# Kernel tuning notes

Measured on AMD Instinct MI355X. Metric: run time of the kernel, lower is better.

## Reference

```python
import jax, jax.numpy as jnp
import numpy as np

H = 128          # input spatial size forced by hardcoded reshape (8 * 16)
BATCH = 128
BLK = 8          # block_size
SUB = 16         # out_channels (sub-frames)
WIN = 3          # window


def setup_inputs() -> dict:
    key = jax.random.key(0)
    k1, k2 = jax.random.split(key, 2)
    coded = jax.random.normal(k1, (BATCH, 1, H, H), dtype=jnp.float32)
    # Conv3d weight: [out=16*64, in/groups=1, kD=9, 1, 1]; kaiming-like scale sqrt(2/9)
    weight = jax.random.normal(k2, (SUB * BLK * BLK, 1, WIN * WIN, 1, 1), dtype=jnp.float32) * np.sqrt(2.0 / 9.0).astype(np.float32)
    bias = jnp.zeros((SUB * BLK * BLK,), dtype=jnp.float32)
    return {"coded": coded, "weight": weight, "bias": bias}


def reference(coded, weight, bias):
    N = coded.shape[0]
    # --- window_shuffle: conv with 3x3 identity filters, pad 1 == 9 shifted copies ---
    pad = jnp.pad(coded, ((0, 0), (0, 0), (1, 1), (1, 1)))  # [N,1,H+2,H+2]
    patches = jnp.stack(
        [pad[:, 0, i:i + H, j:j + H] for i in range(WIN) for j in range(WIN)],
        axis=1,
    )  # [N,9,H,H]
    # --- reverse_pixel_shuffle (space-to-depth, block 8), vectorized over the 9 channels ---
    Hs = H // BLK  # 16
    x = patches.reshape(N, WIN * WIN, Hs, BLK, Hs, BLK)
    x = x.transpose(0, 1, 3, 5, 2, 4).reshape(N, WIN * WIN, BLK * BLK, Hs, Hs)
    x = x.transpose(0, 2, 1, 3, 4)  # [N,64,9,16,16] (torch.stack dim=2 order)
    # --- depthwise Conv3d: groups=64, kernel (9,1,1) -> per-group 9-tap dot ---
    W = weight.reshape(BLK * BLK, SUB, WIN * WIN)  # [64,16,9]
    b = bias.reshape(BLK * BLK, SUB)               # [64,16]
    out = jnp.einsum('ngihw,gmi->ngmhw', x, W) + b[None, :, :, None, None]  # [N,64,16,16,16]
    # --- reshape/transpose/pixel-shuffle ---
    out = out.transpose(0, 2, 1, 3, 4).reshape(N, SUB * BLK * BLK, Hs, Hs)  # [N,1024,16,16]
    out = out.reshape(N, SUB, BLK, BLK, Hs, Hs)
    out = out.transpose(0, 1, 4, 2, 5, 3).reshape(N, SUB, H, H)  # [N,16,128,128]
    return out
```

## Files before the change

### kernel.cpp

```cpp
#include <hip/hip_runtime.h>


#define H 128
#define N_BATCH 128
#define SUB 16

__global__ __launch_bounds__(256, 4) void shiftconv_kernel(
        const float* __restrict__ x,
        const float* __restrict__ w,
        const float* __restrict__ bias,
        float* __restrict__ out) {
    int bid = blockIdx.x;
    int nlo = bid & 7;
    int q   = bid >> 3;
    int mh  = q & 1;
    int b1  = (q >> 1) & 7;
    int n   = ((q >> 4) << 3) | nlo;

    __shared__ float ws[8 * 80];
    {
        int t = threadIdx.x;
        if (t < 64) {
            int mi = t >> 3;
            int h  = (t >> 2) & 1;
            int jj = t & 3;
            int oc = (b1 * 8 + 4 * h + jj) * 16 + (mh * 8 + mi);
            float* dst = ws + mi * 80 + h * 40;
            const float* src = w + oc * 9;
#pragma unroll
            for (int i = 0; i < 9; ++i) dst[i * 4 + jj] = src[i];
            dst[36 + jj] = bias[oc];
        }
    }

    int c  = threadIdx.x & 31;
    int r  = threadIdx.x >> 5;
    int x0 = c << 2;
    int h  = c & 1;
    int y0 = b1 + (r << 3);

    const float* xn = x + (size_t)n * (H * H);

    float in[2][3][6];
#pragma unroll
    for (int g = 0; g < 2; ++g) {
        int yg = y0 + (g << 6);
#pragma unroll
        for (int dy = 0; dy < 3; ++dy) {
            int ry = yg + dy - 1;
            float4 a = make_float4(0.0f, 0.0f, 0.0f, 0.0f);
            if (ry >= 0 && ry < H) a = *(const float4*)(xn + ry * H + x0);
            in[g][dy][1] = a.x; in[g][dy][2] = a.y;
            in[g][dy][3] = a.z; in[g][dy][4] = a.w;
            float left  = __shfl_up(a.w, 1);
            float right = __shfl_down(a.x, 1);
            in[g][dy][0] = (c == 0)  ? 0.0f : left;
            in[g][dy][5] = (c == 31) ? 0.0f : right;
        }
    }

    __syncthreads();

    float* ob = out + ((size_t)(n * SUB + mh * 8)) * (H * H) + y0 * H + x0;

#pragma unroll
    for (int mi = 0; mi < 8; ++mi) {
        const float4* wp = (const float4*)(ws + mi * 80 + h * 40);
        float4 b4 = wp[9];
        float a0[4] = {b4.x, b4.y, b4.z, b4.w};
        float a1[4] = {b4.x, b4.y, b4.z, b4.w};
#pragma unroll
        for (int dy = 0; dy < 3; ++dy) {
#pragma unroll
            for (int dj = 0; dj < 3; ++dj) {
                float4 w4 = wp[dy * 3 + dj];
                a0[0] = fmaf(in[0][dy][dj + 0], w4.x, a0[0]);
                a0[1] = fmaf(in[0][dy][dj + 1], w4.y, a0[1]);
                a0[2] = fmaf(in[0][dy][dj + 2], w4.z, a0[2]);
                a0[3] = fmaf(in[0][dy][dj + 3], w4.w, a0[3]);
                a1[0] = fmaf(in[1][dy][dj + 0], w4.x, a1[0]);
                a1[1] = fmaf(in[1][dy][dj + 1], w4.y, a1[1]);
                a1[2] = fmaf(in[1][dy][dj + 2], w4.z, a1[2]);
                a1[3] = fmaf(in[1][dy][dj + 3], w4.w, a1[3]);
            }
        }
        float* p = ob + (size_t)mi * (H * H);
        *(float4*)(p)          = make_float4(a0[0], a0[1], a0[2], a0[3]);
        *(float4*)(p + 64 * H) = make_float4(a1[0], a1[1], a1[2], a1[3]);
    }
}

extern "C" void kernel_launch(void* const* d_in, const int* in_sizes, int n_in,
                              void* d_out, int out_size, void* d_ws, size_t ws_size,
                              hipStream_t stream) {
    const float* coded  = (const float*)d_in[0];
    const float* weight = (const float*)d_in[1];
    const float* bias   = (const float*)d_in[2];
    float* out = (float*)d_out;

    shiftconv_kernel<<<N_BATCH * 8 * 2, 256, 0, stream>>>(coded, weight, bias, out);
}
```

Measured before the change: 146.1 us.

## Prepack weights in a prep kernel and give each block contiguous rows

A small prep kernel repacks the weights and bias once into a workspace in the per-thread float4 layout. The main kernel then copies all 8 row-phase weight sets with coalesced float4 loads instead of scattered scalar gathers. Each block now covers 8 contiguous rows rather than rows strided by 8, so input loads and output stores are more contiguous. The costs are an extra kernel launch, larger shared memory per block (20KB), and each warp reading a different weight slice.

```diff
diff --git a/kernel.cpp b/kernel.cpp
--- a/kernel.cpp
+++ b/kernel.cpp
@@ -5,39 +5,48 @@
 #define N_BATCH 128
 #define SUB 16
 
+__global__ void wprep_kernel(const float* __restrict__ w,
+                             const float* __restrict__ bias,
+                             float* __restrict__ Wt) {
+    int t = blockIdx.x * blockDim.x + threadIdx.x;
+    if (t >= 1024) return;
+    int jj = t & 3;
+    int h  = (t >> 2) & 1;
+    int mi = (t >> 3) & 7;
+    int b1 = (t >> 6) & 7;
+    int mh = (t >> 9) & 1;
+    int oc = (b1 * 8 + 4 * h + jj) * 16 + mh * 8 + mi;
+    float* dst = Wt + ((mh * 8 + b1) * 8 + mi) * 80 + h * 40;
+#pragma unroll
+    for (int i = 0; i < 9; ++i) dst[i * 4 + jj] = w[oc * 9 + i];
+    dst[36 + jj] = bias[oc];
+}
+
 __global__ __launch_bounds__(256, 4) void shiftconv_kernel(
         const float* __restrict__ x,
-        const float* __restrict__ w,
-        const float* __restrict__ bias,
+        const float* __restrict__ Wt,
         float* __restrict__ out) {
     int bid = blockIdx.x;
     int nlo = bid & 7;
     int q   = bid >> 3;
     int mh  = q & 1;
-    int b1  = (q >> 1) & 7;
+    int k0  = (q >> 1) & 7;
     int n   = ((q >> 4) << 3) | nlo;
 
-    __shared__ float ws[8 * 80];
+    __shared__ float ws[8 * 8 * 80];
     {
         int t = threadIdx.x;
-        if (t < 64) {
-            int mi = t >> 3;
-            int h  = (t >> 2) & 1;
-            int jj = t & 3;
-            int oc = (b1 * 8 + 4 * h + jj) * 16 + (mh * 8 + mi);
-            float* dst = ws + mi * 80 + h * 40;
-            const float* src = w + oc * 9;
+        const float4* src = (const float4*)(Wt + mh * (8 * 8 * 80));
+        float4* dst = (float4*)ws;
 #pragma unroll
-            for (int i = 0; i < 9; ++i) dst[i * 4 + jj] = src[i];
-            dst[36 + jj] = bias[oc];
-        }
+        for (int i = 0; i < 5; ++i) dst[t + 256 * i] = src[t + 256 * i];
     }
 
     int c  = threadIdx.x & 31;
     int r  = threadIdx.x >> 5;
     int x0 = c << 2;
     int h  = c & 1;
-    int y0 = b1 + (r << 3);
+    int y0 = (k0 << 3) + r;
 
     const float* xn = x + (size_t)n * (H * H);
 
@@ -62,10 +71,11 @@
     __syncthreads();
 
     float* ob = out + ((size_t)(n * SUB + mh * 8)) * (H * H) + y0 * H + x0;
+    const float* wbase = ws + (r * 8) * 80 + h * 40;
 
 #pragma unroll
     for (int mi = 0; mi < 8; ++mi) {
-        const float4* wp = (const float4*)(ws + mi * 80 + h * 40);
+        const float4* wp = (const float4*)(wbase + mi * 80);
         float4 b4 = wp[9];
         float a0[4] = {b4.x, b4.y, b4.z, b4.w};
         float a1[4] = {b4.x, b4.y, b4.z, b4.w};
@@ -97,6 +107,8 @@
     const float* weight = (const float*)d_in[1];
     const float* bias   = (const float*)d_in[2];
     float* out = (float*)d_out;
+    float* Wt  = (float*)d_ws;
 
-    shiftconv_kernel<<<N_BATCH * 8 * 2, 256, 0, stream>>>(coded, weight, bias, out);
+    wprep_kernel<<<4, 256, 0, stream>>>(weight, bias, Wt);
+    shiftconv_kernel<<<N_BATCH * 2 * 8, 256, 0, stream>>>(coded, Wt, out);
 }
```

After: 155.1 us. +6.2%, slower.
